# Kernel tuning notes

Hardware: AMD Instinct MI355X
Metric: run time of the kernel (lower is better)

## Reference

```python
import jax, jax.numpy as jnp
import numpy as np

STRIDE = 1
PADDING = 1
DILATION = 1


def _conv_one(xi, wi):
    # xi: [C_in, H, W], wi: [C_out, C_in, ks, ks]
    out = jax.lax.conv_general_dilated(
        xi[None],  # [1, C_in, H, W]
        wi,
        window_strides=(STRIDE, STRIDE),
        padding=[(PADDING, PADDING), (PADDING, PADDING)],
        rhs_dilation=(DILATION, DILATION),
        dimension_numbers=("NCHW", "OIHW", "NCHW"),
    )
    return out[0]  # [C_out, H', W']


def setup_inputs() -> dict:
    key = jax.random.key(0)
    k1, k2, k3 = jax.random.split(key, 3)
    B, C_in, C_out, H, W, ks = 32, 32, 32, 256, 256, 3
    x = jax.random.normal(k1, (B, C_in, H, W), dtype=jnp.float32)
    weight = jax.random.normal(k2, (B, C_out, C_in, ks, ks), dtype=jnp.float32)
    bias = jax.random.normal(k3, (B, C_out), dtype=jnp.float32)
    return {"x": x, "weight": weight, "bias": bias}


def reference(x, weight, bias):
    # Per-sample conv: sample i of x convolved with weight[i].
    out = jax.vmap(_conv_one)(x, weight)  # [B, C_out, H', W']
    out = out + bias[:, :, None, None]
    return out
```

## Files before the change

kernel.cpp:

```cpp
#include <hip/hip_runtime.h>


#define BB 32
#define CI 32
#define CO 32
#define HH 256
#define WW 256

typedef unsigned int uint;
using short8  = __attribute__((ext_vector_type(8))) short;
using float4v = __attribute__((ext_vector_type(4))) float;

__device__ inline unsigned short f2bf(float f) {
    union { float f; uint u; } c; c.f = f;
    uint r = c.u + 0x7fffu + ((c.u >> 16) & 1u);
    return (unsigned short)(r >> 16);
}

__global__ __launch_bounds__(256)
void transpose_kernel(const float* __restrict__ x,
                      unsigned short* __restrict__ xt) {
    __shared__ float tile[CI * 260];
    const int h = blockIdx.x;
    const int b = blockIdx.y;
    const int t = threadIdx.x;

    const float* xp = x + (size_t)b * CI * HH * WW + (size_t)h * WW;
    #pragma unroll
    for (int i = 0; i < 8; ++i) {
        int idx = t + 256 * i;
        int w4  = idx & 63;
        int ci  = idx >> 6;
        float4 v = *(const float4*)(xp + (size_t)ci * HH * WW + w4 * 4);
        *(float4*)(&tile[ci * 260 + w4 * 4]) = v;
    }
    __syncthreads();

    const int w = t;
    uint dw[16];
    #pragma unroll
    for (int j = 0; j < 16; ++j) {
        uint lo = f2bf(tile[(2 * j) * 260 + w]);
        uint hi = f2bf(tile[(2 * j + 1) * 260 + w]);
        dw[j] = lo | (hi << 16);
    }
    unsigned short* op = xt + (((size_t)(b * HH + h)) * WW + w) * CI;
    #pragma unroll
    for (int q = 0; q < 4; ++q) {
        uint4 v = make_uint4(dw[4*q+0], dw[4*q+1], dw[4*q+2], dw[4*q+3]);
        *(uint4*)(op + q * 8) = v;
    }
}

__global__ __launch_bounds__(256)
void wconv_kernel(const float* __restrict__ wgt,
                  unsigned short* __restrict__ wb) {
    const int i = blockIdx.x * 256 + threadIdx.x;
    const int bc  = i / 288;
    const int rem = i - bc * 288;
    const int ci  = rem / 9;
    const int tap = rem - ci * 9;
    wb[(bc * 9 + tap) * CI + ci] = f2bf(wgt[i]);
}

#define TH 8
#define TW 32
#define XR (TH + 2)
#define XC (TW + 2)

__device__ inline int swz_us(int pix, int q) {
    return pix * CI + (((q ^ (pix >> 1)) & 3) << 3);
}

__global__ __launch_bounds__(256)
void conv_mfma_kernel(const unsigned short* __restrict__ xt,
                      const unsigned short* __restrict__ wb,
                      const float* __restrict__ bias,
                      float* __restrict__ out) {
    __shared__ __align__(16) unsigned short xs[XR * XC * CI];

    const int tw = blockIdx.x;
    const int th = blockIdx.y;
    const int b  = blockIdx.z;
    const int t  = threadIdx.x;
    const int h0 = th * TH, w0 = tw * TW;

    const int wv  = t >> 6;
    const int l   = t & 63;
    const int lp  = l & 15;
    const int lq  = l >> 4;

    const unsigned short* wbb = wb + (size_t)(b * CO) * 9 * CI;
    short8 A0[9], A1[9];
    #pragma unroll
    for (int tp = 0; tp < 9; ++tp) {
        A0[tp] = *(const short8*)(wbb + ((lp)      * 9 + tp) * CI + lq * 8);
        A1[tp] = *(const short8*)(wbb + ((16 + lp) * 9 + tp) * CI + lq * 8);
    }

    for (int i = t; i < XR * XC * 4; i += 256) {
        int q   = i & 3;
        int pix = i >> 2;
        int r   = pix / XC;
        int c   = pix - r * XC;
        int h   = h0 - 1 + r;
        int w   = w0 - 1 + c;
        uint4 v = make_uint4(0, 0, 0, 0);
        if (h >= 0 && h < HH && w >= 0 && w < WW) {
            v = *(const uint4*)(xt + (((size_t)(b * HH + h)) * WW + w) * CI + q * 8);
        }
        *(uint4*)(&xs[swz_us(pix, q)]) = v;
    }
    __syncthreads();

    float4v acc0[4], acc1[4];
    #pragma unroll
    for (int g = 0; g < 4; ++g) {
        acc0[g] = {0.f, 0.f, 0.f, 0.f};
        acc1[g] = {0.f, 0.f, 0.f, 0.f};
    }

    #pragma unroll
    for (int g = 0; g < 4; ++g) {
        const int gg = wv * 4 + g;
        const int r  = gg >> 1;
        const int c0 = (gg & 1) * 16;
        #pragma unroll
        for (int kh = 0; kh < 3; ++kh) {
            #pragma unroll
            for (int kw = 0; kw < 3; ++kw) {
                const int p = (r + kh) * XC + (c0 + lp + kw);
                short8 Bf = *(const short8*)(&xs[swz_us(p, lq)]);
                acc0[g] = __builtin_amdgcn_mfma_f32_16x16x32_bf16(
                    A0[kh * 3 + kw], Bf, acc0[g], 0, 0, 0);
                acc1[g] = __builtin_amdgcn_mfma_f32_16x16x32_bf16(
                    A1[kh * 3 + kw], Bf, acc1[g], 0, 0, 0);
            }
        }
    }

    float bv0[4], bv1[4];
    #pragma unroll
    for (int v = 0; v < 4; ++v) {
        bv0[v] = bias[b * CO + lq * 4 + v];
        bv1[v] = bias[b * CO + 16 + lq * 4 + v];
    }

    #pragma unroll
    for (int g = 0; g < 4; ++g) {
        const int gg = wv * 4 + g;
        const int r  = gg >> 1;
        const int c0 = (gg & 1) * 16;
        const int h  = h0 + r;
        const int wpix = w0 + c0 + lp;
        #pragma unroll
        for (int v = 0; v < 4; ++v) {
            const int co_l = lq * 4 + v;
            out[(((size_t)(b * CO + co_l)) * HH + h) * WW + wpix] =
                acc0[g][v] + bv0[v];
            out[(((size_t)(b * CO + 16 + co_l)) * HH + h) * WW + wpix] =
                acc1[g][v] + bv1[v];
        }
    }
}

#define FHT 16
#define FXR (FHT + 2)
#define LROW 264

__global__ __launch_bounds__(256)
void conv3x3_fallback(const float* __restrict__ x,
                      const float* __restrict__ wgt,
                      const float* __restrict__ bias,
                      float* __restrict__ out) {
    __shared__ float xs[FXR * LROW];
    __shared__ float wsh[CI * 9];
    const int co = blockIdx.x;
    const int ht = blockIdx.y;
    const int b  = blockIdx.z;
    const int tid = threadIdx.x;
    const int h0 = ht * FHT;
    for (int i = tid; i < CI * 9; i += 256)
        wsh[i] = wgt[((size_t)(b * CO + co) * CI) * 9 + i];
    for (int i = tid; i < FXR * 8; i += 256) {
        int row = i >> 3; int c = i & 7;
        int col = (c < 4) ? c : (256 + c);
        xs[row * LROW + col] = 0.0f;
    }
    const int wg = tid & 63, rp = tid >> 6;
    const int w0 = wg * 4, r0 = rp * 4;
    float acc[4][4];
    #pragma unroll
    for (int d = 0; d < 4; ++d)
        #pragma unroll
        for (int j = 0; j < 4; ++j) acc[d][j] = 0.0f;
    const float* xb = x + (size_t)(b * CI) * HH * WW;
    for (int ci = 0; ci < CI; ++ci) {
        __syncthreads();
        const float* xsrc = xb + (size_t)ci * HH * WW;
        for (int i = tid; i < FXR * 64; i += 256) {
            int row = i >> 6; int cq = i & 63;
            int gh = h0 - 1 + row;
            float4 v = make_float4(0.f, 0.f, 0.f, 0.f);
            if (gh >= 0 && gh < HH)
                v = *(const float4*)(xsrc + (size_t)gh * WW + cq * 4);
            *(float4*)(&xs[row * LROW + 4 + cq * 4]) = v;
        }
        __syncthreads();
        float wk[9];
        #pragma unroll
        for (int k = 0; k < 9; ++k) wk[k] = wsh[ci * 9 + k];
        #pragma unroll
        for (int xr = 0; xr < 6; ++xr) {
            const float* rowp = &xs[(r0 + xr) * LROW + w0];
            float xv[12];
            #pragma unroll
            for (int q = 0; q < 3; ++q) {
                float4 v = *(const float4*)(rowp + 4 * q);
                xv[4*q+0] = v.x; xv[4*q+1] = v.y; xv[4*q+2] = v.z; xv[4*q+3] = v.w;
            }
            #pragma unroll
            for (int dr = 0; dr < 4; ++dr) {
                const int kh = xr - dr;
                if (kh < 0 || kh > 2) continue;
                #pragma unroll
                for (int kw = 0; kw < 3; ++kw) {
                    const float wvv = wk[kh * 3 + kw];
                    #pragma unroll
                    for (int j = 0; j < 4; ++j)
                        acc[dr][j] += xv[j + kw + 3] * wvv;
                }
            }
        }
    }
    const float bv = bias[b * CO + co];
    float* ob = out + ((size_t)(b * CO + co) * HH + (h0 + r0)) * WW + w0;
    #pragma unroll
    for (int dr = 0; dr < 4; ++dr) {
        float4 o;
        o.x = acc[dr][0] + bv; o.y = acc[dr][1] + bv;
        o.z = acc[dr][2] + bv; o.w = acc[dr][3] + bv;
        *(float4*)(ob + (size_t)dr * WW) = o;
    }
}

extern "C" void kernel_launch(void* const* d_in, const int* in_sizes, int n_in,
                              void* d_out, int out_size, void* d_ws, size_t ws_size,
                              hipStream_t stream) {
    const float* x    = (const float*)d_in[0];
    const float* wgt  = (const float*)d_in[1];
    const float* bias = (const float*)d_in[2];
    float* out        = (float*)d_out;

    const size_t xt_elems = (size_t)BB * HH * WW * CI;
    const size_t wb_elems = (size_t)BB * CO * 9 * CI;
    const size_t need = (xt_elems + wb_elems) * sizeof(unsigned short);
    if (ws_size >= need) {
        unsigned short* xtp = (unsigned short*)d_ws;
        unsigned short* wbp = xtp + xt_elems;
        hipLaunchKernelGGL(transpose_kernel, dim3(HH, BB), dim3(256), 0, stream,
                           x, xtp);
        hipLaunchKernelGGL(wconv_kernel, dim3((BB * CO * CI * 9) / 256), dim3(256),
                           0, stream, wgt, wbp);
        hipLaunchKernelGGL(conv_mfma_kernel, dim3(WW / TW, HH / TH, BB), dim3(256),
                           0, stream, xtp, wbp, bias, out);
    } else {
        hipLaunchKernelGGL(conv3x3_fallback, dim3(CO, HH / FHT, BB), dim3(256),
                           0, stream, x, wgt, bias, out);
    }
}
```

Baseline: 546.6 us.

## Fuse NCHW-to-NHWC bf16 transpose into conv tile load, drop separate pass

Removes the standalone transpose kernel that wrote a bf16 NHWC copy of the input to workspace. The conv kernel now reads fp32 NCHW directly in float4 chunks, pairs two channels, converts them to bf16 and writes them into the swizzled shared-memory tile. This avoids a full extra round trip through global memory for the input. In exchange the tile load re-reads halo columns as fp32, and the LDS stores shrink to 4-byte scattered writes.

```diff
diff --git a/kernel.cpp b/kernel.cpp
--- a/kernel.cpp
+++ b/kernel.cpp
@@ -15,41 +15,6 @@
     union { float f; uint u; } c; c.f = f;
     uint r = c.u + 0x7fffu + ((c.u >> 16) & 1u);
     return (unsigned short)(r >> 16);
-}
-
-__global__ __launch_bounds__(256)
-void transpose_kernel(const float* __restrict__ x,
-                      unsigned short* __restrict__ xt) {
-    __shared__ float tile[CI * 260];
-    const int h = blockIdx.x;
-    const int b = blockIdx.y;
-    const int t = threadIdx.x;
-
-    const float* xp = x + (size_t)b * CI * HH * WW + (size_t)h * WW;
-    #pragma unroll
-    for (int i = 0; i < 8; ++i) {
-        int idx = t + 256 * i;
-        int w4  = idx & 63;
-        int ci  = idx >> 6;
-        float4 v = *(const float4*)(xp + (size_t)ci * HH * WW + w4 * 4);
-        *(float4*)(&tile[ci * 260 + w4 * 4]) = v;
-    }
-    __syncthreads();
-
-    const int w = t;
-    uint dw[16];
-    #pragma unroll
-    for (int j = 0; j < 16; ++j) {
-        uint lo = f2bf(tile[(2 * j) * 260 + w]);
-        uint hi = f2bf(tile[(2 * j + 1) * 260 + w]);
-        dw[j] = lo | (hi << 16);
-    }
-    unsigned short* op = xt + (((size_t)(b * HH + h)) * WW + w) * CI;
-    #pragma unroll
-    for (int q = 0; q < 4; ++q) {
-        uint4 v = make_uint4(dw[4*q+0], dw[4*q+1], dw[4*q+2], dw[4*q+3]);
-        *(uint4*)(op + q * 8) = v;
-    }
 }
 
 __global__ __launch_bounds__(256)
@@ -73,10 +38,10 @@
 }
 
 __global__ __launch_bounds__(256)
-void conv_mfma_kernel(const unsigned short* __restrict__ xt,
-                      const unsigned short* __restrict__ wb,
-                      const float* __restrict__ bias,
-                      float* __restrict__ out) {
+void conv_fused_kernel(const float* __restrict__ x,
+                       const unsigned short* __restrict__ wb,
+                       const float* __restrict__ bias,
+                       float* __restrict__ out) {
     __shared__ __align__(16) unsigned short xs[XR * XC * CI];
 
     const int tw = blockIdx.x;
@@ -98,18 +63,34 @@
         A1[tp] = *(const short8*)(wbb + ((16 + lp) * 9 + tp) * CI + lq * 8);
     }
 
-    for (int i = t; i < XR * XC * 4; i += 256) {
-        int q   = i & 3;
-        int pix = i >> 2;
-        int r   = pix / XC;
-        int c   = pix - r * XC;
-        int h   = h0 - 1 + r;
-        int w   = w0 - 1 + c;
-        uint4 v = make_uint4(0, 0, 0, 0);
-        if (h >= 0 && h < HH && w >= 0 && w < WW) {
-            v = *(const uint4*)(xt + (((size_t)(b * HH + h)) * WW + w) * CI + q * 8);
-        }
-        *(uint4*)(&xs[swz_us(pix, q)]) = v;
+    const float* xb = x + (size_t)b * CI * HH * WW;
+    for (int i = t; i < 1600; i += 256) {
+        const int f   = i % 10;
+        const int rr  = (i / 10) % 10;
+        const int ci2 = i / 100;
+        const int ci  = ci2 * 2;
+        const int h   = h0 - 1 + rr;
+        const int c4  = w0 - 4 + 4 * f;
+        float4 va = make_float4(0.f, 0.f, 0.f, 0.f);
+        float4 vc = make_float4(0.f, 0.f, 0.f, 0.f);
+        if (h >= 0 && h < HH && c4 >= 0 && c4 < WW) {
+            const float* p0 = xb + (size_t)ci * HH * WW + (size_t)h * WW + c4;
+            va = *(const float4*)p0;
+            vc = *(const float4*)(p0 + (size_t)HH * WW);
+        }
+        const float ae[4] = {va.x, va.y, va.z, va.w};
+        const float ce[4] = {vc.x, vc.y, vc.z, vc.w};
+        #pragma unroll
+        for (int e = 0; e < 4; ++e) {
+            const int cl = 4 * f + e - 3;
+            if (cl >= 0 && cl < XC) {
+                const int p = rr * XC + cl;
+                const uint val = (uint)f2bf(ae[e]) | ((uint)f2bf(ce[e]) << 16);
+                const int idx = p * CI + (((ci >> 3) ^ ((p >> 1) & 3)) << 3)
+                              + (ci & 7);
+                *(uint*)(&xs[idx]) = val;
+            }
+        }
     }
     __syncthreads();
 
@@ -252,18 +233,13 @@
     const float* bias = (const float*)d_in[2];
     float* out        = (float*)d_out;
 
-    const size_t xt_elems = (size_t)BB * HH * WW * CI;
-    const size_t wb_elems = (size_t)BB * CO * 9 * CI;
-    const size_t need = (xt_elems + wb_elems) * sizeof(unsigned short);
-    if (ws_size >= need) {
-        unsigned short* xtp = (unsigned short*)d_ws;
-        unsigned short* wbp = xtp + xt_elems;
-        hipLaunchKernelGGL(transpose_kernel, dim3(HH, BB), dim3(256), 0, stream,
-                           x, xtp);
+    const size_t wb_bytes = (size_t)BB * CO * 9 * CI * sizeof(unsigned short);
+    if (ws_size >= wb_bytes) {
+        unsigned short* wbp = (unsigned short*)d_ws;
         hipLaunchKernelGGL(wconv_kernel, dim3((BB * CO * CI * 9) / 256), dim3(256),
                            0, stream, wgt, wbp);
-        hipLaunchKernelGGL(conv_mfma_kernel, dim3(WW / TW, HH / TH, BB), dim3(256),
-                           0, stream, xtp, wbp, bias, out);
+        hipLaunchKernelGGL(conv_fused_kernel, dim3(WW / TW, HH / TH, BB), dim3(256),
+                           0, stream, x, wbp, bias, out);
     } else {
         hipLaunchKernelGGL(conv3x3_fallback, dim3(CO, HH / FHT, BB), dim3(256),
                            0, stream, x, wgt, bias, out);
```

New measurement: 503.5 us. 7.9% less time.
